# Optimization experiments

Hardware: AMD Instinct MI355X
Metric: run time of the kernel (lower is better)

The kernel has to match this reference:

```python
import jax, jax.numpy as jnp
import numpy as np

EMBED_DIM = 1024
N_HEADS = 16
HEAD_DIM = EMBED_DIM // N_HEADS
EPS = 1e-6


def setup_inputs() -> dict:
    key = jax.random.key(0)
    k_x, k_wqkv, k_bqkv, k_wo, k_bo = jax.random.split(key, 5)
    B, T, C = 2, 2048, EMBED_DIM
    s = 1.0 / np.sqrt(C)
    return {
        "x": jax.random.normal(k_x, (B, T, C), dtype=jnp.float32),
        "w_qkv": jax.random.normal(k_wqkv, (C, 3 * C), dtype=jnp.float32) * s,
        "b_qkv": jax.random.normal(k_bqkv, (3 * C,), dtype=jnp.float32) * s,
        "w_out": jax.random.normal(k_wo, (C, C), dtype=jnp.float32) * s,
        "b_out": jax.random.normal(k_bo, (C,), dtype=jnp.float32) * s,
    }


def reference(x, w_qkv, b_qkv, w_out, b_out):
    B, T, C = x.shape
    H, D = N_HEADS, HEAD_DIM
    qkv = x @ w_qkv + b_qkv                       # [B,T,3C]
    q, k, v = jnp.split(qkv, 3, axis=-1)
    # [B,H,T,D]
    q = q.reshape(B, T, H, D).transpose(0, 2, 1, 3)
    k = k.reshape(B, T, H, D).transpose(0, 2, 1, 3)
    v = v.reshape(B, T, H, D).transpose(0, 2, 1, 3)
    dot = jnp.einsum("bhqd,bhkd->bhqk", q, k)     # [B,H,T,T]
    q_sq = jnp.sum(q * q, axis=-1)[..., :, None]  # [B,H,T,1]
    k_sq = jnp.sum(k * k, axis=-1)[..., None, :]  # [B,H,1,T]
    scores = (dot * dot) / (q_sq + k_sq - 2.0 * dot + EPS)
    causal = jnp.tril(jnp.ones((T, T), dtype=bool))
    scores = jnp.where(causal, scores, -jnp.inf)
    attn = jax.nn.softmax(scores, axis=-1)
    out = jnp.einsum("bhqk,bhkd->bhqd", attn, v)  # [B,H,T,D]
    out = out.transpose(0, 2, 1, 3).reshape(B, T, C)
    return out @ w_out + b_out
```

## Files before the change

kernel.cpp:

```cpp
#include <hip/hip_runtime.h>
#include <stdint.h>


#define TSEQ 2048
#define BATCH 2

typedef _Float16 f16x8 __attribute__((ext_vector_type(8)));
typedef __fp16 fp16x2 __attribute__((ext_vector_type(2)));
typedef float f32x4 __attribute__((ext_vector_type(4)));
typedef unsigned int u32x2 __attribute__((ext_vector_type(2)));

#define MFMA16(a, b, c) __builtin_amdgcn_mfma_f32_16x16x32_f16(a, b, c, 0, 0, 0)

__device__ __forceinline__ unsigned short f2h(float f) {
  union { _Float16 h; unsigned short u; } v;
  v.h = (_Float16)f;
  return v.u;
}
__device__ __forceinline__ float h2f(unsigned short u) {
  union { unsigned short u; _Float16 h; } v;
  v.u = u;
  return (float)v.h;
}
__device__ __forceinline__ unsigned int pack2h(float lo, float hi) {
  return (unsigned int)f2h(lo) | ((unsigned int)f2h(hi) << 16);
}
__device__ __forceinline__ float sumsq_u32(unsigned int u) {
  float lo = h2f(u & 0xffffu);
  float hi = h2f(u >> 16);
  return lo * lo + hi * hi;
}
__device__ __forceinline__ void async_ld16(const void* g, const void* l) {
  __builtin_amdgcn_global_load_lds((const __attribute__((address_space(1))) void*)g,
                                   (__attribute__((address_space(3))) void*)l,
                                   16, 0, 0);
}
__device__ __forceinline__ unsigned int pk_f16(float lo, float hi) {
  union { fp16x2 h; unsigned int u; } c;
  c.h = __builtin_amdgcn_cvt_pkrtz(lo, hi);
  return c.u;
}

__global__ __launch_bounds__(256) void cvt_x(const float* __restrict__ src,
                                             unsigned short* __restrict__ dst) {
  const int i = (blockIdx.x * 256 + threadIdx.x) * 8;
  const float4 a = *(const float4*)(src + i);
  const float4 b = *(const float4*)(src + i + 4);
  uint4 o;
  o.x = pack2h(a.x, a.y); o.y = pack2h(a.z, a.w);
  o.z = pack2h(b.x, b.y); o.w = pack2h(b.z, b.w);
  *(uint4*)(dst + i) = o;
}

__global__ __launch_bounds__(256) void transpose_w(const float* __restrict__ src,
                                                   unsigned short* __restrict__ dst,
                                                   int K, int N) {
  __shared__ unsigned short tile[32][33];
  const int tx = threadIdx.x, ty = threadIdx.y;
  const int nb = blockIdx.x * 32, kb = blockIdx.y * 32;
#pragma unroll
  for (int i = 0; i < 4; i++)
    tile[ty + 8 * i][tx] = f2h(src[(size_t)(kb + ty + 8 * i) * N + nb + tx]);
  __syncthreads();
#pragma unroll
  for (int i = 0; i < 4; i++)
    dst[(size_t)(nb + ty + 8 * i) * K + kb + tx] = tile[tx][ty + 8 * i];
}

template <int TN, bool OUT_F32>
__global__ __launch_bounds__(256) void gemm_bt(const unsigned short* __restrict__ A,
                                               const unsigned short* __restrict__ Bt,
                                               const float* __restrict__ bias,
                                               void* __restrict__ Cp,
                                               int N, int K) {
  __shared__ __attribute__((aligned(16))) unsigned short Atile[128 * 32];
  __shared__ __attribute__((aligned(16))) unsigned short Btile[TN * 32];
  constexpr int NJ = TN / 32;
  const int tid = threadIdx.x;
  const int w = tid >> 6, lane = tid & 63;
  const int quad = lane >> 4, l15 = lane & 15;
  const int m0 = blockIdx.y * 128, n0 = blockIdx.x * TN;
  const int wr = w >> 1, wc = w & 1;
  const int nwc = wc * (TN / 2);
  f32x4 acc[4][NJ] = {};
  for (int kt = 0; kt < K; kt += 32) {
    __syncthreads();
#pragma unroll
    for (int it = 0; it < 2; it++) {
      const int c = it * 256 + tid;
      async_ld16(A + (size_t)(m0 + (c >> 2)) * K + kt + (c & 3) * 8,
                 &Atile[(size_t)(it * 256 + w * 64) * 8]);
    }
#pragma unroll
    for (int it = 0; it < TN / 64; it++) {
      const int c = it * 256 + tid;
      async_ld16(Bt + (size_t)(n0 + (c >> 2)) * K + kt + (c & 3) * 8,
                 &Btile[(size_t)(it * 256 + w * 64) * 8]);
    }
    __syncthreads();
    f16x8 af[4], bfr[NJ];
#pragma unroll
    for (int i = 0; i < 4; i++)
      af[i] = *(const f16x8*)&Atile[(wr * 64 + i * 16 + l15) * 32 + quad * 8];
#pragma unroll
    for (int j = 0; j < NJ; j++)
      bfr[j] = *(const f16x8*)&Btile[(nwc + j * 16 + l15) * 32 + quad * 8];
#pragma unroll
    for (int i = 0; i < 4; i++)
#pragma unroll
      for (int j = 0; j < NJ; j++)
        acc[i][j] = MFMA16(af[i], bfr[j], acc[i][j]);
  }
#pragma unroll
  for (int j = 0; j < NJ; j++) {
    const int n = n0 + nwc + j * 16 + l15;
    const float bv = bias[n];
#pragma unroll
    for (int i = 0; i < 4; i++) {
      const int mb = m0 + wr * 64 + i * 16 + quad * 4;
#pragma unroll
      for (int r = 0; r < 4; r++) {
        if constexpr (OUT_F32)
          ((float*)Cp)[(size_t)(mb + r) * N + n] = acc[i][j][r] + bv;
        else
          ((unsigned short*)Cp)[(size_t)(mb + r) * N + n] = f2h(acc[i][j][r] + bv);
      }
    }
  }
}

__global__ __launch_bounds__(256, 4) void yat_attn(const unsigned short* __restrict__ qkv,
                                                   unsigned short* __restrict__ outp) {
  __shared__ __attribute__((aligned(16))) unsigned short Qp[64 * 72];
  __shared__ __attribute__((aligned(16))) unsigned short Kp[64 * 72];
  __shared__ __attribute__((aligned(16))) unsigned short Vt[64 * 72];
  __shared__ float qsq[64], ksq[64];
  const int tid = threadIdx.x;
  const int w = tid >> 6, lane = tid & 63;
  const int quad = lane >> 4, l15 = lane & 15;
  const int bh = blockIdx.x, b = bh >> 4, h = bh & 15;
  const int y = blockIdx.y;
  const int qt = (y < 8) ? 31 - y : (y < 16) ? y - 8 : (y < 24) ? 39 - y : y - 16;
  const unsigned short* base = qkv + (size_t)b * TSEQ * 3072 + h * 64;
  const int t = tid >> 2, dc = (tid & 3) * 16;
  const int d0 = tid & 31, tg8 = tid >> 5;

  {
    const unsigned short* g = base + (size_t)(qt * 64 + t) * 3072 + dc;
    uint4 v0 = *(const uint4*)g;
    uint4 v1 = *(const uint4*)(g + 8);
    *(uint4*)&Qp[t * 72 + dc] = v0;
    *(uint4*)&Qp[t * 72 + dc + 8] = v1;
    float s = sumsq_u32(v0.x) + sumsq_u32(v0.y) + sumsq_u32(v0.z) + sumsq_u32(v0.w) +
              sumsq_u32(v1.x) + sumsq_u32(v1.y) + sumsq_u32(v1.z) + sumsq_u32(v1.w);
    s += __shfl_xor(s, 1);
    s += __shfl_xor(s, 2);
    if ((tid & 3) == 0) qsq[t] = s;
  }
  __syncthreads();
  const f16x8 aq0 = *(const f16x8*)&Qp[(w * 16 + l15) * 72 + quad * 8];
  const f16x8 aq1 = *(const f16x8*)&Qp[(w * 16 + l15) * 72 + 32 + quad * 8];
  const f16x8 onesf = {(_Float16)1.f, (_Float16)1.f, (_Float16)1.f, (_Float16)1.f,
                       (_Float16)1.f, (_Float16)1.f, (_Float16)1.f, (_Float16)1.f};
  const int ql = w * 16 + l15;
  const float qsq_eps = qsq[ql] + 1e-6f;

  f32x4 accO[4] = {};
  float m_run = 0.f;
  float l_acc = 0.f;

  uint4 kreg0, kreg1;
  unsigned int vreg[8];
  {
    const unsigned short* gk = base + 1024 + (size_t)t * 3072 + dc;
    kreg0 = *(const uint4*)gk;
    kreg1 = *(const uint4*)(gk + 8);
    const unsigned short* gv = base + 2048 + (size_t)(tg8 * 8) * 3072 + 2 * d0;
#pragma unroll
    for (int s = 0; s < 8; s++)
      vreg[s] = *(const unsigned int*)(gv + (size_t)s * 3072);
  }

  for (int kt = 0; kt <= qt; kt++) {
    __syncthreads();
    {
      *(uint4*)&Kp[t * 72 + dc] = kreg0;
      *(uint4*)&Kp[t * 72 + dc + 8] = kreg1;
      float s = sumsq_u32(kreg0.x) + sumsq_u32(kreg0.y) + sumsq_u32(kreg0.z) +
                sumsq_u32(kreg0.w) + sumsq_u32(kreg1.x) + sumsq_u32(kreg1.y) +
                sumsq_u32(kreg1.z) + sumsq_u32(kreg1.w);
      s += __shfl_xor(s, 1);
      s += __shfl_xor(s, 2);
      if ((tid & 3) == 0) ksq[t] = s;
      uint4 LO, HI;
      LO.x = (vreg[0] & 0xffffu) | (vreg[1] << 16);
      LO.y = (vreg[2] & 0xffffu) | (vreg[3] << 16);
      LO.z = (vreg[4] & 0xffffu) | (vreg[5] << 16);
      LO.w = (vreg[6] & 0xffffu) | (vreg[7] << 16);
      HI.x = (vreg[0] >> 16) | (vreg[1] & 0xffff0000u);
      HI.y = (vreg[2] >> 16) | (vreg[3] & 0xffff0000u);
      HI.z = (vreg[4] >> 16) | (vreg[5] & 0xffff0000u);
      HI.w = (vreg[6] >> 16) | (vreg[7] & 0xffff0000u);
      *(uint4*)&Vt[(2 * d0) * 72 + tg8 * 8] = LO;
      *(uint4*)&Vt[(2 * d0 + 1) * 72 + tg8 * 8] = HI;
    }
    if (kt < qt) {
      const unsigned short* gk = base + 1024 + (size_t)((kt + 1) * 64 + t) * 3072 + dc;
      kreg0 = *(const uint4*)gk;
      kreg1 = *(const uint4*)(gk + 8);
      const unsigned short* gv =
          base + 2048 + (size_t)((kt + 1) * 64 + tg8 * 8) * 3072 + 2 * d0;
#pragma unroll
      for (int s = 0; s < 8; s++)
        vreg[s] = *(const unsigned int*)(gv + (size_t)s * 3072);
    }
    __syncthreads();

    f32x4 accS[4] = {};
#pragma unroll
    for (int nt = 0; nt < 4; nt++) {
      const f16x8 bk0 = *(const f16x8*)&Kp[(nt * 16 + l15) * 72 + quad * 8];
      const f16x8 bk1 = *(const f16x8*)&Kp[(nt * 16 + l15) * 72 + 32 + quad * 8];
      accS[nt] = MFMA16(bk0, aq0, accS[nt]);
      accS[nt] = MFMA16(bk1, aq1, accS[nt]);
    }
    float pv[4][4];
#pragma unroll
    for (int nt = 0; nt < 4; nt++) {
      const f32x4 k4 = *(const f32x4*)&ksq[nt * 16 + quad * 4];
#pragma unroll
      for (int r = 0; r < 4; r++) {
        const float d = accS[nt][r];
        const float den = __builtin_fmaf(-2.f, d, k4[r] + qsq_eps);
        pv[nt][r] = d * d * __builtin_amdgcn_rcpf(den);
      }
    }
    if (kt == qt) {
#pragma unroll
      for (int nt = 0; nt < 4; nt++)
#pragma unroll
        for (int r = 0; r < 4; r++)
          if (nt * 16 + quad * 4 + r > ql) pv[nt][r] = -1e30f;
    }
    float tm = fmaxf(fmaxf(fmaxf(pv[0][0], pv[0][1]), fmaxf(pv[0][2], pv[0][3])),
                     fmaxf(fmaxf(pv[1][0], pv[1][1]), fmaxf(pv[1][2], pv[1][3])));
    tm = fmaxf(tm, fmaxf(fmaxf(fmaxf(pv[2][0], pv[2][1]), fmaxf(pv[2][2], pv[2][3])),
                         fmaxf(fmaxf(pv[3][0], pv[3][1]), fmaxf(pv[3][2], pv[3][3]))));
    tm = fmaxf(tm, __shfl_xor(tm, 16));
    tm = fmaxf(tm, __shfl_xor(tm, 32));
    const float mn = fmaxf(m_run, tm);
    const float alpha = __expf(m_run - mn);
    m_run = mn;
    unsigned int pa[4], pb[4];
#pragma unroll
    for (int nt = 0; nt < 4; nt++) {
      pa[nt] = pk_f16(__expf(pv[nt][0] - mn), __expf(pv[nt][1] - mn));
      pb[nt] = pk_f16(__expf(pv[nt][2] - mn), __expf(pv[nt][3] - mn));
    }
    union { f16x8 v; unsigned int u[4]; } bp0, bp1;
    {
      u32x2 s0 = __builtin_amdgcn_permlane32_swap(pa[0], pa[1], false, false);
      u32x2 s1 = __builtin_amdgcn_permlane16_swap(s0.x, s0.y, false, false);
      bp0.u[0] = s1.x; bp0.u[2] = s1.y;
      s0 = __builtin_amdgcn_permlane32_swap(pb[0], pb[1], false, false);
      s1 = __builtin_amdgcn_permlane16_swap(s0.x, s0.y, false, false);
      bp0.u[1] = s1.x; bp0.u[3] = s1.y;
      s0 = __builtin_amdgcn_permlane32_swap(pa[2], pa[3], false, false);
      s1 = __builtin_amdgcn_permlane16_swap(s0.x, s0.y, false, false);
      bp1.u[0] = s1.x; bp1.u[2] = s1.y;
      s0 = __builtin_amdgcn_permlane32_swap(pb[2], pb[3], false, false);
      s1 = __builtin_amdgcn_permlane16_swap(s0.x, s0.y, false, false);
      bp1.u[1] = s1.x; bp1.u[3] = s1.y;
    }
#pragma unroll
    for (int i = 0; i < 4; i++) {
      accO[i][0] *= alpha; accO[i][1] *= alpha;
      accO[i][2] *= alpha; accO[i][3] *= alpha;
    }
    f32x4 accL = {};
    accL = MFMA16(onesf, bp0.v, accL);
    accL = MFMA16(onesf, bp1.v, accL);
#pragma unroll
    for (int i = 0; i < 4; i++) {
      const f16x8 av0 = *(const f16x8*)&Vt[(i * 16 + l15) * 72 + quad * 8];
      const f16x8 av1 = *(const f16x8*)&Vt[(i * 16 + l15) * 72 + 32 + quad * 8];
      accO[i] = MFMA16(av0, bp0.v, accO[i]);
      accO[i] = MFMA16(av1, bp1.v, accO[i]);
    }
    l_acc = l_acc * alpha + accL[0];
  }

  __syncthreads();
  const float linv = 1.0f / l_acc;
#pragma unroll
  for (int i = 0; i < 4; i++)
#pragma unroll
    for (int r = 0; r < 4; r++)
      Qp[(w * 16 + l15) * 72 + i * 16 + quad * 4 + r] = f2h(accO[i][r] * linv);
  __syncthreads();
  {
    uint4 o0 = *(const uint4*)&Qp[t * 72 + dc];
    uint4 o1 = *(const uint4*)&Qp[t * 72 + dc + 8];
    unsigned short* g = outp + (size_t)(b * TSEQ + qt * 64 + t) * 1024 + h * 64 + dc;
    *(uint4*)g = o0;
    *(uint4*)(g + 8) = o1;
  }
}

extern "C" void kernel_launch(void* const* d_in, const int* in_sizes, int n_in,
                              void* d_out, int out_size, void* d_ws, size_t ws_size,
                              hipStream_t stream) {
  (void)in_sizes; (void)n_in; (void)out_size; (void)ws_size;
  const float* x     = (const float*)d_in[0];
  const float* w_qkv = (const float*)d_in[1];
  const float* b_qkv = (const float*)d_in[2];
  const float* w_out = (const float*)d_in[3];
  const float* b_out = (const float*)d_in[4];
  float* out = (float*)d_out;

  unsigned short* wqkvT  = (unsigned short*)d_ws;
  unsigned short* woT    = wqkvT + (size_t)3072 * 1024;
  unsigned short* qkvws  = woT + (size_t)1024 * 1024;
  unsigned short* xh     = qkvws + (size_t)4096 * 3072;
  unsigned short* attnws = xh;

  cvt_x<<<dim3(4096 * 1024 / (256 * 8)), 256, 0, stream>>>(x, xh);
  transpose_w<<<dim3(3072 / 32, 1024 / 32), dim3(32, 8), 0, stream>>>(w_qkv, wqkvT, 1024, 3072);
  transpose_w<<<dim3(1024 / 32, 1024 / 32), dim3(32, 8), 0, stream>>>(w_out, woT, 1024, 1024);
  gemm_bt<128, false><<<dim3(3072 / 128, 4096 / 128), 256, 0, stream>>>(xh, wqkvT, b_qkv, qkvws, 3072, 1024);
  yat_attn<<<dim3(BATCH * 16, 32), 256, 0, stream>>>(qkvws, attnws);
  gemm_bt<64, true><<<dim3(1024 / 64, 4096 / 128), 256, 0, stream>>>(attnws, woT, b_out, out, 1024, 1024);
}
```

Baseline: 195.8 us.

## Double-buffer K/V shared tiles in attention to drop one barrier per tile

```diff
diff --git a/kernel.cpp b/kernel.cpp
--- a/kernel.cpp
+++ b/kernel.cpp
@@ -131,10 +131,9 @@
 
 __global__ __launch_bounds__(256, 4) void yat_attn(const unsigned short* __restrict__ qkv,
                                                    unsigned short* __restrict__ outp) {
-  __shared__ __attribute__((aligned(16))) unsigned short Qp[64 * 72];
-  __shared__ __attribute__((aligned(16))) unsigned short Kp[64 * 72];
-  __shared__ __attribute__((aligned(16))) unsigned short Vt[64 * 72];
-  __shared__ float qsq[64], ksq[64];
+  __shared__ __attribute__((aligned(16))) unsigned short Kp[2][64 * 72];
+  __shared__ __attribute__((aligned(16))) unsigned short Vt[2][64 * 72];
+  __shared__ float qsq[64], ksq[2][64];
   const int tid = threadIdx.x;
   const int w = tid >> 6, lane = tid & 63;
   const int quad = lane >> 4, l15 = lane & 15;
@@ -145,30 +144,6 @@
   const int t = tid >> 2, dc = (tid & 3) * 16;
   const int d0 = tid & 31, tg8 = tid >> 5;
 
-  {
-    const unsigned short* g = base + (size_t)(qt * 64 + t) * 3072 + dc;
-    uint4 v0 = *(const uint4*)g;
-    uint4 v1 = *(const uint4*)(g + 8);
-    *(uint4*)&Qp[t * 72 + dc] = v0;
-    *(uint4*)&Qp[t * 72 + dc + 8] = v1;
-    float s = sumsq_u32(v0.x) + sumsq_u32(v0.y) + sumsq_u32(v0.z) + sumsq_u32(v0.w) +
-              sumsq_u32(v1.x) + sumsq_u32(v1.y) + sumsq_u32(v1.z) + sumsq_u32(v1.w);
-    s += __shfl_xor(s, 1);
-    s += __shfl_xor(s, 2);
-    if ((tid & 3) == 0) qsq[t] = s;
-  }
-  __syncthreads();
-  const f16x8 aq0 = *(const f16x8*)&Qp[(w * 16 + l15) * 72 + quad * 8];
-  const f16x8 aq1 = *(const f16x8*)&Qp[(w * 16 + l15) * 72 + 32 + quad * 8];
-  const f16x8 onesf = {(_Float16)1.f, (_Float16)1.f, (_Float16)1.f, (_Float16)1.f,
-                       (_Float16)1.f, (_Float16)1.f, (_Float16)1.f, (_Float16)1.f};
-  const int ql = w * 16 + l15;
-  const float qsq_eps = qsq[ql] + 1e-6f;
-
-  f32x4 accO[4] = {};
-  float m_run = 0.f;
-  float l_acc = 0.f;
-
   uint4 kreg0, kreg1;
   unsigned int vreg[8];
   {
@@ -180,54 +155,76 @@
     for (int s = 0; s < 8; s++)
       vreg[s] = *(const unsigned int*)(gv + (size_t)s * 3072);
   }
+  {
+    const unsigned short* g = base + (size_t)(qt * 64 + t) * 3072 + dc;
+    uint4 v0 = *(const uint4*)g;
+    uint4 v1 = *(const uint4*)(g + 8);
+    *(uint4*)&Kp[1][t * 72 + dc] = v0;
+    *(uint4*)&Kp[1][t * 72 + dc + 8] = v1;
+    float s = sumsq_u32(v0.x) + sumsq_u32(v0.y) + sumsq_u32(v0.z) + sumsq_u32(v0.w) +
+              sumsq_u32(v1.x) + sumsq_u32(v1.y) + sumsq_u32(v1.z) + sumsq_u32(v1.w);
+    s += __shfl_xor(s, 1);
+    s += __shfl_xor(s, 2);
+    if ((tid & 3) == 0) qsq[t] = s;
+  }
+  auto commit = [&](int buf) {
+    *(uint4*)&Kp[buf][t * 72 + dc] = kreg0;
+    *(uint4*)&Kp[buf][t * 72 + dc + 8] = kreg1;
+    float s = sumsq_u32(kreg0.x) + sumsq_u32(kreg0.y) + sumsq_u32(kreg0.z) +
+              sumsq_u32(kreg0.w) + sumsq_u32(kreg1.x) + sumsq_u32(kreg1.y) +
+              sumsq_u32(kreg1.z) + sumsq_u32(kreg1.w);
+    s += __shfl_xor(s, 1);
+    s += __shfl_xor(s, 2);
+    if ((tid & 3) == 0) ksq[buf][t] = s;
+    uint4 LO, HI;
+    LO.x = (vreg[0] & 0xffffu) | (vreg[1] << 16);
+    LO.y = (vreg[2] & 0xffffu) | (vreg[3] << 16);
+    LO.z = (vreg[4] & 0xffffu) | (vreg[5] << 16);
+    LO.w = (vreg[6] & 0xffffu) | (vreg[7] << 16);
+    HI.x = (vreg[0] >> 16) | (vreg[1] & 0xffff0000u);
+    HI.y = (vreg[2] >> 16) | (vreg[3] & 0xffff0000u);
+    HI.z = (vreg[4] >> 16) | (vreg[5] & 0xffff0000u);
+    HI.w = (vreg[6] >> 16) | (vreg[7] & 0xffff0000u);
+    *(uint4*)&Vt[buf][(2 * d0) * 72 + tg8 * 8] = LO;
+    *(uint4*)&Vt[buf][(2 * d0 + 1) * 72 + tg8 * 8] = HI;
+  };
+  commit(0);
+  if (qt >= 1) {
+    const unsigned short* gk = base + 1024 + (size_t)(64 + t) * 3072 + dc;
+    kreg0 = *(const uint4*)gk;
+    kreg1 = *(const uint4*)(gk + 8);
+    const unsigned short* gv = base + 2048 + (size_t)(64 + tg8 * 8) * 3072 + 2 * d0;
+#pragma unroll
+    for (int s = 0; s < 8; s++)
+      vreg[s] = *(const unsigned int*)(gv + (size_t)s * 3072);
+  }
+  __syncthreads();
+  const f16x8 aq0 = *(const f16x8*)&Kp[1][(w * 16 + l15) * 72 + quad * 8];
+  const f16x8 aq1 = *(const f16x8*)&Kp[1][(w * 16 + l15) * 72 + 32 + quad * 8];
+  const f16x8 onesf = {(_Float16)1.f, (_Float16)1.f, (_Float16)1.f, (_Float16)1.f,
+                       (_Float16)1.f, (_Float16)1.f, (_Float16)1.f, (_Float16)1.f};
+  const int ql = w * 16 + l15;
+  const float qsq_eps = qsq[ql] + 1e-6f;
+  __syncthreads();
+
+  f32x4 accO[4] = {};
+  float m_run = 0.f;
+  float l_acc = 0.f;
 
   for (int kt = 0; kt <= qt; kt++) {
-    __syncthreads();
-    {
-      *(uint4*)&Kp[t * 72 + dc] = kreg0;
-      *(uint4*)&Kp[t * 72 + dc + 8] = kreg1;
-      float s = sumsq_u32(kreg0.x) + sumsq_u32(kreg0.y) + sumsq_u32(kreg0.z) +
-                sumsq_u32(kreg0.w) + sumsq_u32(kreg1.x) + sumsq_u32(kreg1.y) +
-                sumsq_u32(kreg1.z) + sumsq_u32(kreg1.w);
-      s += __shfl_xor(s, 1);
-      s += __shfl_xor(s, 2);
-      if ((tid & 3) == 0) ksq[t] = s;
-      uint4 LO, HI;
-      LO.x = (vreg[0] & 0xffffu) | (vreg[1] << 16);
-      LO.y = (vreg[2] & 0xffffu) | (vreg[3] << 16);
-      LO.z = (vreg[4] & 0xffffu) | (vreg[5] << 16);
-      LO.w = (vreg[6] & 0xffffu) | (vreg[7] << 16);
-      HI.x = (vreg[0] >> 16) | (vreg[1] & 0xffff0000u);
-      HI.y = (vreg[2] >> 16) | (vreg[3] & 0xffff0000u);
-      HI.z = (vreg[4] >> 16) | (vreg[5] & 0xffff0000u);
-      HI.w = (vreg[6] >> 16) | (vreg[7] & 0xffff0000u);
-      *(uint4*)&Vt[(2 * d0) * 72 + tg8 * 8] = LO;
-      *(uint4*)&Vt[(2 * d0 + 1) * 72 + tg8 * 8] = HI;
-    }
-    if (kt < qt) {
-      const unsigned short* gk = base + 1024 + (size_t)((kt + 1) * 64 + t) * 3072 + dc;
-      kreg0 = *(const uint4*)gk;
-      kreg1 = *(const uint4*)(gk + 8);
-      const unsigned short* gv =
-          base + 2048 + (size_t)((kt + 1) * 64 + tg8 * 8) * 3072 + 2 * d0;
-#pragma unroll
-      for (int s = 0; s < 8; s++)
-        vreg[s] = *(const unsigned int*)(gv + (size_t)s * 3072);
-    }
-    __syncthreads();
-
+    const int cur = kt & 1;
     f32x4 accS[4] = {};
 #pragma unroll
     for (int nt = 0; nt < 4; nt++) {
-      const f16x8 bk0 = *(const f16x8*)&Kp[(nt * 16 + l15) * 72 + quad * 8];
-      const f16x8 bk1 = *(const f16x8*)&Kp[(nt * 16 + l15) * 72 + 32 + quad * 8];
+      const f16x8 bk0 = *(const f16x8*)&Kp[cur][(nt * 16 + l15) * 72 + quad * 8];
+      const f16x8 bk1 = *(const f16x8*)&Kp[cur][(nt * 16 + l15) * 72 + 32 + quad * 8];
       accS[nt] = MFMA16(bk0, aq0, accS[nt]);
       accS[nt] = MFMA16(bk1, aq1, accS[nt]);
     }
     float pv[4][4];
 #pragma unroll
     for (int nt = 0; nt < 4; nt++) {
-      const f32x4 k4 = *(const f32x4*)&ksq[nt * 16 + quad * 4];
+      const f32x4 k4 = *(const f32x4*)&ksq[cur][nt * 16 + quad * 4];
 #pragma unroll
       for (int r = 0; r < 4; r++) {
         const float d = accS[nt][r];
@@ -256,6 +253,17 @@
     for (int nt = 0; nt < 4; nt++) {
       pa[nt] = pk_f16(__expf(pv[nt][0] - mn), __expf(pv[nt][1] - mn));
       pb[nt] = pk_f16(__expf(pv[nt][2] - mn), __expf(pv[nt][3] - mn));
+    }
+    if (kt < qt) commit(cur ^ 1);
+    if (kt + 2 <= qt) {
+      const unsigned short* gk = base + 1024 + (size_t)((kt + 2) * 64 + t) * 3072 + dc;
+      kreg0 = *(const uint4*)gk;
+      kreg1 = *(const uint4*)(gk + 8);
+      const unsigned short* gv =
+          base + 2048 + (size_t)((kt + 2) * 64 + tg8 * 8) * 3072 + 2 * d0;
+#pragma unroll
+      for (int s = 0; s < 8; s++)
+        vreg[s] = *(const unsigned int*)(gv + (size_t)s * 3072);
     }
     union { f16x8 v; unsigned int u[4]; } bp0, bp1;
     {
@@ -282,25 +290,25 @@
     accL = MFMA16(onesf, bp1.v, accL);
 #pragma unroll
     for (int i = 0; i < 4; i++) {
-      const f16x8 av0 = *(const f16x8*)&Vt[(i * 16 + l15) * 72 + quad * 8];
-      const f16x8 av1 = *(const f16x8*)&Vt[(i * 16 + l15) * 72 + 32 + quad * 8];
+      const f16x8 av0 = *(const f16x8*)&Vt[cur][(i * 16 + l15) * 72 + quad * 8];
+      const f16x8 av1 = *(const f16x8*)&Vt[cur][(i * 16 + l15) * 72 + 32 + quad * 8];
       accO[i] = MFMA16(av0, bp0.v, accO[i]);
       accO[i] = MFMA16(av1, bp1.v, accO[i]);
     }
     l_acc = l_acc * alpha + accL[0];
-  }
-
-  __syncthreads();
+    __syncthreads();
+  }
+
   const float linv = 1.0f / l_acc;
 #pragma unroll
   for (int i = 0; i < 4; i++)
 #pragma unroll
     for (int r = 0; r < 4; r++)
-      Qp[(w * 16 + l15) * 72 + i * 16 + quad * 4 + r] = f2h(accO[i][r] * linv);
+      Kp[0][(w * 16 + l15) * 72 + i * 16 + quad * 4 + r] = f2h(accO[i][r] * linv);
   __syncthreads();
   {
-    uint4 o0 = *(const uint4*)&Qp[t * 72 + dc];
-    uint4 o1 = *(const uint4*)&Qp[t * 72 + dc + 8];
+    uint4 o0 = *(const uint4*)&Kp[0][t * 72 + dc];
+    uint4 o1 = *(const uint4*)&Kp[0][t * 72 + dc + 8];
     unsigned short* g = outp + (size_t)(b * TSEQ + qt * 64 + t) * 1024 + h * 64 + dc;
     *(uint4*)g = o0;
     *(uint4*)(g + 8) = o1;
```

New measurement: 194.8 us. No clear change (-0.5%).
